# Performance work log

Measured on AMD Instinct MI355X. Metric: run time of the kernel, lower is better.

The kernel has to match this reference:

```python
import jax, jax.numpy as jnp
import numpy as np

INPUT_SIZE = 1024
HIDDEN_SIZE = 2048
BATCH = 4096


def _xavier(key, shape):
    fan_out, fan_in = shape
    std = jnp.sqrt(2.0 / (fan_in + fan_out)).astype(jnp.float32)
    return jax.random.normal(key, shape, dtype=jnp.float32) * std


def setup_inputs() -> dict:
    key = jax.random.key(0)
    ks = jax.random.split(key, 8)
    return {
        "x": jax.random.normal(ks[0], (BATCH, INPUT_SIZE), dtype=jnp.float32),
        "hprev": jax.random.normal(ks[1], (BATCH, HIDDEN_SIZE), dtype=jnp.float32),
        "Wh": _xavier(ks[2], (HIDDEN_SIZE, INPUT_SIZE)),
        "Wz": _xavier(ks[3], (HIDDEN_SIZE, INPUT_SIZE)),
        "Wr": _xavier(ks[4], (HIDDEN_SIZE, INPUT_SIZE)),
        "Uh": _xavier(ks[5], (HIDDEN_SIZE, HIDDEN_SIZE)),
        "Uz": _xavier(ks[6], (HIDDEN_SIZE, HIDDEN_SIZE)),
        "Ur": _xavier(ks[7], (HIDDEN_SIZE, HIDDEN_SIZE)),
        "bh": jnp.zeros((HIDDEN_SIZE,), dtype=jnp.float32),
        "bz": jnp.zeros((HIDDEN_SIZE,), dtype=jnp.float32),
        "br": jnp.zeros((HIDDEN_SIZE,), dtype=jnp.float32),
    }


def reference(x, hprev, Wh, Wz, Wr, Uh, Uz, Ur, bh, bz, br):
    # batched matvec: (b,i) @ (h,i)^T -> (b,h)
    r = jax.nn.sigmoid(x @ Wr.T + hprev @ Ur.T + br)
    z = jax.nn.sigmoid(x @ Wz.T + hprev @ Uz.T + bz)
    h_proposed = jnp.tanh(x @ Wh.T + (r * hprev) @ Uh.T + bh)
    return z * h_proposed + (1.0 - z) * hprev
```

## Files before the change

### kernel.cpp

```cpp
#include <hip/hip_runtime.h>

#define BATCH 4096
#define ISZ   1024
#define HSZ   2048

typedef __bf16 bf16x8 __attribute__((ext_vector_type(8)));
typedef float  f32x4  __attribute__((ext_vector_type(4)));

__device__ __forceinline__ unsigned short f2bf(float f) {
  unsigned u = __builtin_bit_cast(unsigned, f);
  u += 0x7fffu + ((u >> 16) & 1u);
  return (unsigned short)(u >> 16);
}
__device__ __forceinline__ float bf2f(unsigned short s) {
  unsigned u = ((unsigned)s) << 16;
  return __builtin_bit_cast(float, u);
}

struct CvtArgs {
  const float* src[8];
  unsigned short* dst[8];
  int cum[9];
};

__global__ __launch_bounds__(256) void cvt_all_kernel(CvtArgs a, int total4) {
  int i = blockIdx.x * 256 + threadIdx.x;
  if (i >= total4) return;
  int s = 0;
#pragma unroll
  for (int k = 0; k < 7; ++k) s += (i >= a.cum[k + 1]) ? 1 : 0;
  int off = i - a.cum[s];
  float4 f = ((const float4*)a.src[s])[off];
  ushort4 o;
  o.x = f2bf(f.x); o.y = f2bf(f.y); o.z = f2bf(f.z); o.w = f2bf(f.w);
  ((ushort4*)a.dst[s])[off] = o;
}

__device__ __forceinline__ void stage_tile64(const unsigned short* __restrict__ g, int ldK,
                                             int tileRow, int k0, char* lds, int t) {
  char* l0 = lds + ((t >> 6) << 10);
#pragma unroll
  for (int k = 0; k < 4; ++k) {
    int linear = t + k * 256;
    int row = linear >> 3;
    int cs  = linear & 7;
    int c   = cs ^ (row & 7);
    const unsigned short* gp = g + (size_t)(tileRow + row) * ldK + (k0 + c * 8);
    __builtin_amdgcn_global_load_lds((const __attribute__((address_space(1))) void*)gp,
                                     (__attribute__((address_space(3))) void*)(l0 + k * 4096),
                                     16, 0, 0);
  }
}

__device__ __forceinline__ void stage_tileB64(const unsigned short* __restrict__ g, int ldK,
                                              int tileRow, int k0, char* lds, int t) {
  char* l0 = lds + ((t >> 6) << 10);
#pragma unroll
  for (int k = 0; k < 2; ++k) {
    int linear = t + k * 256;
    int row = linear >> 3;
    int cs  = linear & 7;
    int c   = cs ^ (row & 7);
    const unsigned short* gp = g + (size_t)(tileRow + row) * ldK + (k0 + c * 8);
    __builtin_amdgcn_global_load_lds((const __attribute__((address_space(1))) void*)gp,
                                     (__attribute__((address_space(3))) void*)(l0 + k * 4096),
                                     16, 0, 0);
  }
}

__device__ __forceinline__ void gemm_seg(const unsigned short* __restrict__ A,
                                         const unsigned short* __restrict__ W,
                                         int K, int rowBase, int colBase,
                                         char* ldsA, char* ldsB,
                                         f32x4 (&acc)[4][4], int t) {
  const int lane = t & 63;
  const int wid  = t >> 6;
  const int wm   = wid >> 1, wn = wid & 1;
  const int lrow = lane & 15;
  const int quad = lane >> 4;
  const int r7   = lrow & 7;
  for (int k0 = 0; k0 < K; k0 += 64) {
    stage_tile64(A, K, rowBase, k0, ldsA, t);
    stage_tile64(W, K, colBase, k0, ldsB, t);
    __syncthreads();
#pragma unroll
    for (int kk = 0; kk < 2; ++kk) {
      const int swz = (((kk << 2) | quad) ^ r7) * 16;
      bf16x8 af[4], bfr[4];
#pragma unroll
      for (int i = 0; i < 4; ++i) {
        af[i]  = *(const bf16x8*)(ldsA + (wm * 64 + i * 16 + lrow) * 128 + swz);
        bfr[i] = *(const bf16x8*)(ldsB + (wn * 64 + i * 16 + lrow) * 128 + swz);
      }
#pragma unroll
      for (int i = 0; i < 4; ++i)
#pragma unroll
        for (int j = 0; j < 4; ++j)
          acc[i][j] = __builtin_amdgcn_mfma_f32_16x16x32_bf16(af[i], bfr[j], acc[i][j], 0, 0, 0);
    }
    __syncthreads();
  }
}

__device__ __forceinline__ void gemm_seg_h(const unsigned short* __restrict__ A,
                                           const unsigned short* __restrict__ W,
                                           int K, int rowBase, int colBase,
                                           char* ldsA, char* ldsB,
                                           f32x4 (&acc)[4][2], int t) {
  const int lane = t & 63;
  const int wid  = t >> 6;
  const int wm   = wid >> 1, wn = wid & 1;
  const int lrow = lane & 15;
  const int quad = lane >> 4;
  const int r7   = lrow & 7;
  for (int k0 = 0; k0 < K; k0 += 64) {
    stage_tile64(A, K, rowBase, k0, ldsA, t);
    stage_tileB64(W, K, colBase, k0, ldsB, t);
    __syncthreads();
#pragma unroll
    for (int kk = 0; kk < 2; ++kk) {
      const int swz = (((kk << 2) | quad) ^ r7) * 16;
      bf16x8 af[4], bfr[2];
#pragma unroll
      for (int i = 0; i < 4; ++i)
        af[i]  = *(const bf16x8*)(ldsA + (wm * 64 + i * 16 + lrow) * 128 + swz);
#pragma unroll
      for (int j = 0; j < 2; ++j)
        bfr[j] = *(const bf16x8*)(ldsB + (wn * 32 + j * 16 + lrow) * 128 + swz);
#pragma unroll
      for (int i = 0; i < 4; ++i)
#pragma unroll
        for (int j = 0; j < 2; ++j)
          acc[i][j] = __builtin_amdgcn_mfma_f32_16x16x32_bf16(af[i], bfr[j], acc[i][j], 0, 0, 0);
    }
    __syncthreads();
  }
}

__device__ __forceinline__ float fast_sigmoid(float v) {
  return 1.0f / (1.0f + __expf(-v));
}
__device__ __forceinline__ float fast_tanh(float v) {
  float e = __expf(2.0f * v);
  return 1.0f - 2.0f / (e + 1.0f);
}

__global__ __launch_bounds__(256, 4) void gate_rz(
    const unsigned short* __restrict__ xb, const unsigned short* __restrict__ hb,
    const unsigned short* __restrict__ Wr, const unsigned short* __restrict__ Ur,
    const unsigned short* __restrict__ Wz, const unsigned short* __restrict__ Uz,
    const float* __restrict__ br, const float* __restrict__ bz,
    unsigned short* __restrict__ rh, unsigned short* __restrict__ Zbuf) {
  __shared__ char lds[32768];
  char* ldsA = lds;
  char* ldsB = lds + 16384;
  const int t = threadIdx.x;

  int lin = blockIdx.x + (blockIdx.y << 4) + (blockIdx.z << 9);
  int xcd = lin & 7, s = lin >> 3;
  int bx = xcd * 2 + (s & 1);
  int by = (s >> 1) & 31;
  int bz_ = s >> 6;

  const int rowBase = by * 128;
  const int colBase = bx * 128;
  const bool isZ = (bz_ != 0);
  const unsigned short* W = isZ ? Wz : Wr;
  const unsigned short* U = isZ ? Uz : Ur;
  const float* biasP = isZ ? bz : br;

  f32x4 acc[4][4];
#pragma unroll
  for (int i = 0; i < 4; ++i)
#pragma unroll
    for (int j = 0; j < 4; ++j)
      acc[i][j] = (f32x4){0.f, 0.f, 0.f, 0.f};

  gemm_seg(xb, W, ISZ, rowBase, colBase, ldsA, ldsB, acc, t);
  gemm_seg(hb, U, HSZ, rowBase, colBase, ldsA, ldsB, acc, t);

  const int lane = t & 63, wid = t >> 6;
  const int wm = wid >> 1, wn = wid & 1, lrow = lane & 15, quad = lane >> 4;
#pragma unroll
  for (int i = 0; i < 4; ++i) {
#pragma unroll
    for (int j = 0; j < 4; ++j) {
      int col = colBase + wn * 64 + j * 16 + lrow;
      float bv = biasP[col];
#pragma unroll
      for (int r = 0; r < 4; ++r) {
        int row = rowBase + wm * 64 + i * 16 + quad * 4 + r;
        float sg = fast_sigmoid(acc[i][j][r] + bv);
        int idx = row * HSZ + col;
        if (isZ) {
          Zbuf[idx] = f2bf(sg);
        } else {
          rh[idx] = f2bf(sg * bf2f(hb[idx]));
        }
      }
    }
  }
}

__global__ __launch_bounds__(256, 5) void gate_h(
    const unsigned short* __restrict__ xb, const unsigned short* __restrict__ rhb,
    const unsigned short* __restrict__ Wh, const unsigned short* __restrict__ Uh,
    const float* __restrict__ bh, const unsigned short* __restrict__ Zbuf,
    const float* __restrict__ hprev, float* __restrict__ out) {
  __shared__ char lds[24576];
  char* ldsA = lds;
  char* ldsB = lds + 16384;
  const int t = threadIdx.x;

  int lin = blockIdx.x + (blockIdx.y << 5);
  int xcd = lin & 7, s = lin >> 3;
  int bx = xcd * 4 + (s & 3);
  int by = s >> 2;

  const int rowBase = by * 128;
  const int colBase = bx * 64;

  f32x4 acc[4][2];
#pragma unroll
  for (int i = 0; i < 4; ++i)
#pragma unroll
    for (int j = 0; j < 2; ++j)
      acc[i][j] = (f32x4){0.f, 0.f, 0.f, 0.f};

  gemm_seg_h(xb, Wh, ISZ, rowBase, colBase, ldsA, ldsB, acc, t);
  gemm_seg_h(rhb, Uh, HSZ, rowBase, colBase, ldsA, ldsB, acc, t);

  const int lane = t & 63, wid = t >> 6;
  const int wm = wid >> 1, wn = wid & 1, lrow = lane & 15, quad = lane >> 4;
#pragma unroll
  for (int i = 0; i < 4; ++i) {
#pragma unroll
    for (int j = 0; j < 2; ++j) {
      int col = colBase + wn * 32 + j * 16 + lrow;
      float bv = bh[col];
#pragma unroll
      for (int r = 0; r < 4; ++r) {
        int row = rowBase + wm * 64 + i * 16 + quad * 4 + r;
        float hp = fast_tanh(acc[i][j][r] + bv);
        int idx = row * HSZ + col;
        float z = bf2f(Zbuf[idx]);
        float h = hprev[idx];
        out[idx] = h + z * (hp - h);
      }
    }
  }
}

extern "C" void kernel_launch(void* const* d_in, const int* in_sizes, int n_in,
                              void* d_out, int out_size, void* d_ws, size_t ws_size,
                              hipStream_t stream) {
  (void)in_sizes; (void)n_in; (void)out_size; (void)ws_size;
  const float* x     = (const float*)d_in[0];
  const float* hprev = (const float*)d_in[1];
  const float* Wh    = (const float*)d_in[2];
  const float* Wz    = (const float*)d_in[3];
  const float* Wr    = (const float*)d_in[4];
  const float* Uh    = (const float*)d_in[5];
  const float* Uz    = (const float*)d_in[6];
  const float* Ur    = (const float*)d_in[7];
  const float* bh    = (const float*)d_in[8];
  const float* bz    = (const float*)d_in[9];
  const float* br    = (const float*)d_in[10];
  float* out = (float*)d_out;

  char* ws = (char*)d_ws;
  size_t off = 0;
  auto alloc = [&](size_t bytes) { char* p = ws + off; off += bytes; return p; };
  unsigned short* xb  = (unsigned short*)alloc((size_t)BATCH * ISZ * 2);
  unsigned short* hb  = (unsigned short*)alloc((size_t)BATCH * HSZ * 2);
  unsigned short* Wrb = (unsigned short*)alloc((size_t)HSZ * ISZ * 2);
  unsigned short* Wzb = (unsigned short*)alloc((size_t)HSZ * ISZ * 2);
  unsigned short* Whb = (unsigned short*)alloc((size_t)HSZ * ISZ * 2);
  unsigned short* Urb = (unsigned short*)alloc((size_t)HSZ * HSZ * 2);
  unsigned short* Uzb = (unsigned short*)alloc((size_t)HSZ * HSZ * 2);
  unsigned short* Uhb = (unsigned short*)alloc((size_t)HSZ * HSZ * 2);
  unsigned short* rhb = (unsigned short*)alloc((size_t)BATCH * HSZ * 2);
  unsigned short* Zb  = (unsigned short*)alloc((size_t)BATCH * HSZ * 2);

  CvtArgs ca;
  const float* srcs[8]      = {x, hprev, Wr, Wz, Wh, Ur, Uz, Uh};
  unsigned short* dsts[8]   = {xb, hb, Wrb, Wzb, Whb, Urb, Uzb, Uhb};
  int n4s[8] = {BATCH * ISZ / 4, BATCH * HSZ / 4,
                HSZ * ISZ / 4, HSZ * ISZ / 4, HSZ * ISZ / 4,
                HSZ * HSZ / 4, HSZ * HSZ / 4, HSZ * HSZ / 4};
  int cum = 0;
  for (int i = 0; i < 8; ++i) {
    ca.src[i] = srcs[i];
    ca.dst[i] = dsts[i];
    ca.cum[i] = cum;
    cum += n4s[i];
  }
  ca.cum[8] = cum;
  cvt_all_kernel<<<(cum + 255) / 256, 256, 0, stream>>>(ca, cum);

  dim3 gridA(HSZ / 128, BATCH / 128, 2);
  gate_rz<<<gridA, 256, 0, stream>>>(xb, hb, Wrb, Urb, Wzb, Uzb, br, bz, rhb, Zb);

  dim3 gridB(HSZ / 64, BATCH / 128, 1);
  gate_h<<<gridB, 256, 0, stream>>>(xb, rhb, Whb, Uhb, bh, Zb, hprev, out);
}
```

Before: 343.2 us.

## Move Wh/Uh conversion into gate_rz extra blocks; widen gate_h tile to 128x128

The fp32-to-bf16 conversion of Wh and Uh moves out of the up-front conversion kernel and into an extra z-slice of the gate_rz grid, so it runs alongside the r/z GEMMs and the serial conversion pass gets shorter. gate_h now uses 512-thread blocks with 8 waves covering a 128x128 output tile instead of 64 columns, which halves how often the A operand is reloaded. The risks are extra conversion blocks competing with GEMM blocks for the GPU, lower occupancy from the larger blocks, and gate_h having only half as many blocks.

Measured after the change: 340.3 us. About the same (-0.9%).

```diff
diff --git a/kernel.cpp b/kernel.cpp
--- a/kernel.cpp
+++ b/kernel.cpp
@@ -18,9 +18,9 @@
 }
 
 struct CvtArgs {
-  const float* src[8];
-  unsigned short* dst[8];
-  int cum[9];
+  const float* src[6];
+  unsigned short* dst[6];
+  int cum[7];
 };
 
 __global__ __launch_bounds__(256) void cvt_all_kernel(CvtArgs a, int total4) {
@@ -28,7 +28,7 @@
   if (i >= total4) return;
   int s = 0;
 #pragma unroll
-  for (int k = 0; k < 7; ++k) s += (i >= a.cum[k + 1]) ? 1 : 0;
+  for (int k = 0; k < 5; ++k) s += (i >= a.cum[k + 1]) ? 1 : 0;
   int off = i - a.cum[s];
   float4 f = ((const float4*)a.src[s])[off];
   ushort4 o;
@@ -52,18 +52,18 @@
   }
 }
 
-__device__ __forceinline__ void stage_tileB64(const unsigned short* __restrict__ g, int ldK,
-                                              int tileRow, int k0, char* lds, int t) {
+__device__ __forceinline__ void stage_tile64_w8(const unsigned short* __restrict__ g, int ldK,
+                                                int tileRow, int k0, char* lds, int t) {
   char* l0 = lds + ((t >> 6) << 10);
 #pragma unroll
   for (int k = 0; k < 2; ++k) {
-    int linear = t + k * 256;
+    int linear = t + k * 512;
     int row = linear >> 3;
     int cs  = linear & 7;
     int c   = cs ^ (row & 7);
     const unsigned short* gp = g + (size_t)(tileRow + row) * ldK + (k0 + c * 8);
     __builtin_amdgcn_global_load_lds((const __attribute__((address_space(1))) void*)gp,
-                                     (__attribute__((address_space(3))) void*)(l0 + k * 4096),
+                                     (__attribute__((address_space(3))) void*)(l0 + k * 8192),
                                      16, 0, 0);
   }
 }
@@ -102,20 +102,21 @@
   }
 }
 
-__device__ __forceinline__ void gemm_seg_h(const unsigned short* __restrict__ A,
-                                           const unsigned short* __restrict__ W,
-                                           int K, int rowBase, int colBase,
-                                           char* ldsA, char* ldsB,
-                                           f32x4 (&acc)[4][2], int t) {
+__device__ __forceinline__ void gemm_seg8(const unsigned short* __restrict__ A,
+                                          const unsigned short* __restrict__ W,
+                                          int K, int rowBase, int colBase,
+                                          char* ldsA, char* ldsB,
+                                          f32x4 (&acc)[4][2], int t) {
   const int lane = t & 63;
   const int wid  = t >> 6;
-  const int wm   = wid >> 1, wn = wid & 1;
+  const int wm   = wid >> 2;
+  const int wn   = wid & 3;
   const int lrow = lane & 15;
   const int quad = lane >> 4;
   const int r7   = lrow & 7;
   for (int k0 = 0; k0 < K; k0 += 64) {
-    stage_tile64(A, K, rowBase, k0, ldsA, t);
-    stage_tileB64(W, K, colBase, k0, ldsB, t);
+    stage_tile64_w8(A, K, rowBase, k0, ldsA, t);
+    stage_tile64_w8(W, K, colBase, k0, ldsB, t);
     __syncthreads();
 #pragma unroll
     for (int kk = 0; kk < 2; ++kk) {
@@ -150,13 +151,32 @@
     const unsigned short* __restrict__ Wr, const unsigned short* __restrict__ Ur,
     const unsigned short* __restrict__ Wz, const unsigned short* __restrict__ Uz,
     const float* __restrict__ br, const float* __restrict__ bz,
+    const float* __restrict__ Wh32, const float* __restrict__ Uh32,
+    unsigned short* __restrict__ Whb, unsigned short* __restrict__ Uhb,
     unsigned short* __restrict__ rh, unsigned short* __restrict__ Zbuf) {
   __shared__ char lds[32768];
+  const int t = threadIdx.x;
+
+  if (blockIdx.z == 0) {
+    const int NW = (HSZ * ISZ) / 4;
+    const int NU = (HSZ * HSZ) / 4;
+    int tid = (blockIdx.x + (blockIdx.y << 4)) * 256 + t;
+    for (int i = tid; i < NW + NU; i += 512 * 256) {
+      const float4* s4 = (i < NW) ? (const float4*)Wh32 + i
+                                  : (const float4*)Uh32 + (i - NW);
+      ushort4* d4 = (i < NW) ? (ushort4*)Whb + i
+                             : (ushort4*)Uhb + (i - NW);
+      float4 f = *s4;
+      ushort4 o;
+      o.x = f2bf(f.x); o.y = f2bf(f.y); o.z = f2bf(f.z); o.w = f2bf(f.w);
+      *d4 = o;
+    }
+    return;
+  }
+
   char* ldsA = lds;
   char* ldsB = lds + 16384;
-  const int t = threadIdx.x;
-
-  int lin = blockIdx.x + (blockIdx.y << 4) + (blockIdx.z << 9);
+  int lin = blockIdx.x + (blockIdx.y << 4) + ((blockIdx.z - 1) << 9);
   int xcd = lin & 7, s = lin >> 3;
   int bx = xcd * 2 + (s & 1);
   int by = (s >> 1) & 31;
@@ -202,23 +222,23 @@
   }
 }
 
-__global__ __launch_bounds__(256, 5) void gate_h(
+__global__ __launch_bounds__(512, 4) void gate_h(
     const unsigned short* __restrict__ xb, const unsigned short* __restrict__ rhb,
     const unsigned short* __restrict__ Wh, const unsigned short* __restrict__ Uh,
     const float* __restrict__ bh, const unsigned short* __restrict__ Zbuf,
     const float* __restrict__ hprev, float* __restrict__ out) {
-  __shared__ char lds[24576];
+  __shared__ char lds[32768];
   char* ldsA = lds;
   char* ldsB = lds + 16384;
   const int t = threadIdx.x;
 
-  int lin = blockIdx.x + (blockIdx.y << 5);
+  int lin = blockIdx.x + (blockIdx.y << 4);
   int xcd = lin & 7, s = lin >> 3;
-  int bx = xcd * 4 + (s & 3);
-  int by = s >> 2;
+  int bx = xcd * 2 + (s & 1);
+  int by = s >> 1;
 
   const int rowBase = by * 128;
-  const int colBase = bx * 64;
+  const int colBase = bx * 128;
 
   f32x4 acc[4][2];
 #pragma unroll
@@ -227,11 +247,11 @@
     for (int j = 0; j < 2; ++j)
       acc[i][j] = (f32x4){0.f, 0.f, 0.f, 0.f};
 
-  gemm_seg_h(xb, Wh, ISZ, rowBase, colBase, ldsA, ldsB, acc, t);
-  gemm_seg_h(rhb, Uh, HSZ, rowBase, colBase, ldsA, ldsB, acc, t);
+  gemm_seg8(xb, Wh, ISZ, rowBase, colBase, ldsA, ldsB, acc, t);
+  gemm_seg8(rhb, Uh, HSZ, rowBase, colBase, ldsA, ldsB, acc, t);
 
   const int lane = t & 63, wid = t >> 6;
-  const int wm = wid >> 1, wn = wid & 1, lrow = lane & 15, quad = lane >> 4;
+  const int wm = wid >> 2, wn = wid & 3, lrow = lane & 15, quad = lane >> 4;
 #pragma unroll
   for (int i = 0; i < 4; ++i) {
 #pragma unroll
@@ -283,24 +303,25 @@
   unsigned short* Zb  = (unsigned short*)alloc((size_t)BATCH * HSZ * 2);
 
   CvtArgs ca;
-  const float* srcs[8]      = {x, hprev, Wr, Wz, Wh, Ur, Uz, Uh};
-  unsigned short* dsts[8]   = {xb, hb, Wrb, Wzb, Whb, Urb, Uzb, Uhb};
-  int n4s[8] = {BATCH * ISZ / 4, BATCH * HSZ / 4,
-                HSZ * ISZ / 4, HSZ * ISZ / 4, HSZ * ISZ / 4,
-                HSZ * HSZ / 4, HSZ * HSZ / 4, HSZ * HSZ / 4};
+  const float* srcs[6]      = {x, hprev, Wr, Wz, Ur, Uz};
+  unsigned short* dsts[6]   = {xb, hb, Wrb, Wzb, Urb, Uzb};
+  int n4s[6] = {BATCH * ISZ / 4, BATCH * HSZ / 4,
+                HSZ * ISZ / 4, HSZ * ISZ / 4,
+                HSZ * HSZ / 4, HSZ * HSZ / 4};
   int cum = 0;
-  for (int i = 0; i < 8; ++i) {
+  for (int i = 0; i < 6; ++i) {
     ca.src[i] = srcs[i];
     ca.dst[i] = dsts[i];
     ca.cum[i] = cum;
     cum += n4s[i];
   }
-  ca.cum[8] = cum;
+  ca.cum[6] = cum;
   cvt_all_kernel<<<(cum + 255) / 256, 256, 0, stream>>>(ca, cum);
 
-  dim3 gridA(HSZ / 128, BATCH / 128, 2);
-  gate_rz<<<gridA, 256, 0, stream>>>(xb, hb, Wrb, Urb, Wzb, Uzb, br, bz, rhb, Zb);
-
-  dim3 gridB(HSZ / 64, BATCH / 128, 1);
-  gate_h<<<gridB, 256, 0, stream>>>(xb, rhb, Whb, Uhb, bh, Zb, hprev, out);
-}
+  dim3 gridA(HSZ / 128, BATCH / 128, 3);
+  gate_rz<<<gridA, 256, 0, stream>>>(xb, hb, Wrb, Urb, Wzb, Uzb, br, bz,
+                                     Wh, Uh, Whb, Uhb, rhb, Zb);
+
+  dim3 gridB(HSZ / 128, BATCH / 128, 1);
+  gate_h<<<gridB, 512, 0, stream>>>(xb, rhb, Whb, Uhb, bh, Zb, hprev, out);
+}
```
